# Optimization experiments

Hardware: AMD Instinct MI355X
Metric: run time of the kernel (lower is better)

## Reference

```python
import jax, jax.numpy as jnp
import numpy as np

B, S, F = 4, 2048, 1024
D_K = 1024


def setup_inputs() -> dict:
    key = jax.random.key(0)
    ks = jax.random.split(key, 9)
    s_in = 1.0 / np.sqrt(F)
    s_dk = 1.0 / np.sqrt(D_K)
    return {
        "x": jax.random.normal(ks[0], (B, S, F), jnp.float32),
        "Wq": jax.random.normal(ks[1], (F, D_K), jnp.float32) * s_in,
        "bq": jax.random.normal(ks[2], (D_K,), jnp.float32) * s_in,
        "Wk": jax.random.normal(ks[3], (F, D_K), jnp.float32) * s_in,
        "bk": jax.random.normal(ks[4], (D_K,), jnp.float32) * s_in,
        "Wv": jax.random.normal(ks[5], (F, D_K), jnp.float32) * s_in,
        "bv": jax.random.normal(ks[6], (D_K,), jnp.float32) * s_in,
        "Wo": jax.random.normal(ks[7], (D_K, F), jnp.float32) * s_dk,
        "bo": jax.random.normal(ks[8], (F,), jnp.float32) * s_dk,
    }


def reference(x, Wq, bq, Wk, bk, Wv, bv, Wo, bo):
    d_k = Wq.shape[1]
    # init_keys(x): keys/values are projections of the same sequence
    keys = jnp.einsum("bsf,fd->bsd", x, Wk) + bk      # [B,S,d_k]
    values = jnp.einsum("bsf,fd->bsd", x, Wv) + bv    # [B,S,d_k]
    queries = jnp.einsum("bsf,fd->bsd", x, Wq) + bq   # [B,S,d_k]
    # scores[b, q, k] = <queries[b,q], keys[b,k]> / sqrt(d_k)
    scores = jnp.einsum("bqd,bkd->bqk", queries, keys) / jnp.sqrt(
        jnp.asarray(d_k, x.dtype)
    )
    # NOTE: original softmaxes over dim=-2, i.e. over the QUERY axis
    attn = jax.nn.softmax(scores, axis=-2)            # [B,Sq,Sk]
    ctx = jnp.einsum("bqk,bkd->bqd", attn, values)    # [B,S,d_k]
    out = jnp.einsum("bqd,df->bqf", ctx, Wo) + bo     # [B,S,F]
    return out
```

## Files before the change

### kernel.cpp

```cpp
#include <hip/hip_runtime.h>
#include <hip/hip_bf16.h>
#include <cstdint>

typedef __bf16 bf16_t;
typedef __bf16 bf16x8 __attribute__((ext_vector_type(8)));
typedef float  floatx4 __attribute__((ext_vector_type(4)));

typedef const __attribute__((address_space(1))) unsigned int* gptr_t;
typedef __attribute__((address_space(3))) unsigned int* lptr_t;

static __device__ __forceinline__ void gl2lds16(const bf16_t* g, bf16_t* l) {
  __builtin_amdgcn_global_load_lds((gptr_t)g, (lptr_t)l, 16, 0, 0);
}

#define BAR()   asm volatile("s_barrier" ::: "memory")
#define WLGKM() asm volatile("s_waitcnt lgkmcnt(0)" ::: "memory")

template<int HAS_BIAS, int EXP_COLSUM, int SPLIT3>
__global__ __launch_bounds__(512, 2)
void gemm256(const bf16_t* __restrict__ A, const bf16_t* __restrict__ Bt,
             void* __restrict__ Cv,
             const float* __restrict__ b0, const float* __restrict__ b1,
             const float* __restrict__ b2,
             float* __restrict__ L,
             int M, int N, int K, int ldC, float alpha,
             long sA, long sB, long sC,
             long co0, long co1, long co2,
             int mbShift, int ldTv, long sTv)
{
  __shared__ __align__(16) char smemc[131072];

  const int bz = blockIdx.z;
  A  += bz * sA;
  Bt += bz * sB;

  int bx, by;
  {
    const int gx = gridDim.x, gy = gridDim.y;
    const int nwg = gx * gy;
    int id = blockIdx.x + gx * blockIdx.y;
    const int q = nwg >> 3, r = nwg & 7;
    const int xcd = id & 7, o = id >> 3;
    id = (xcd < r ? xcd * (q + 1) : r * (q + 1) + (xcd - r) * q) + o;
    bx = id % gx;
    by = id / gx;
  }

  const int gn0 = bx * 256;
  const int m0  = by * 256;
  const int tid  = threadIdx.x;
  const int lane = tid & 63;
  const int wave = tid >> 6;
  const int wm   = wave >> 2;
  const int wn   = wave & 3;
  const int lm   = lane & 15;
  const int quad = lane >> 4;

  int n0 = gn0, which = 0;
  bf16_t* Cb = (bf16_t*)Cv;
  const float* bias = b0;
  if (SPLIT3) {
    which = gn0 >> 10;
    n0 = gn0 & 1023;
    Cb += (which == 0) ? co0 : (which == 1) ? co1 : co2;
    bias = (which == 0) ? b0 : (which == 1) ? b1 : b2;
  }

  const int srow = tid >> 2;
  const int scol = ((tid ^ (tid >> 3)) & 3) * 8;
  const bf16_t* pA = A  + (long)(m0  + srow) * K + scol;
  const bf16_t* pB = Bt + (long)(gn0 + srow) * K + scol;

  const int nt = K >> 6;

  auto STAGE = [&](int s) {
    if (s >= 4 * nt) return;
    const int ts  = s >> 2;
    const int h   = s & 3;
    const int isA = h & 1;
    const int kh  = h >> 1;
    const bf16_t* gp = (isA ? pA : pB) + ts * 64 + kh * 32;
    char* lp = smemc + (ts & 1) * 65536 + (isA ? 0 : 32768) + kh * 16384
             + tid * 16;
    gl2lds16(gp,                (bf16_t*)lp);
    gl2lds16(gp + (long)128 * K, (bf16_t*)(lp + 8192));
  };

  const int csz  = ((quad ^ (lm >> 1)) & 3) * 16;
  const int aoff = (wm * 128 + lm) * 64 + csz;
  const int boff = (wn * 64  + lm) * 64 + csz;
  auto LDA = [&](int buf, int ks, int f) {
    return *(const bf16x8*)(smemc + buf * 65536 + ks * 16384 + aoff + f * 1024);
  };
  auto LDB = [&](int buf, int ks, int j) {
    return *(const bf16x8*)(smemc + buf * 65536 + 32768 + ks * 16384 + boff
                            + j * 1024);
  };

  floatx4 acc[8][4];
#pragma unroll
  for (int f = 0; f < 8; ++f)
#pragma unroll
    for (int j = 0; j < 4; ++j)
      acc[f][j] = (floatx4)(0.f);

#pragma unroll
  for (int s = 0; s < 7; ++s) STAGE(s);
  asm volatile("s_waitcnt vmcnt(6)" ::: "memory");
  BAR();

  for (int t = 0; t < nt; ++t) {
    const int buf = t & 1;
    bf16x8 a[4], b0r[4], b1r[4];

#pragma unroll
    for (int j = 0; j < 4; ++j) b0r[j] = LDB(buf, 0, j);
#pragma unroll
    for (int f = 0; f < 4; ++f) a[f] = LDA(buf, 0, f);
    STAGE(4 * t + 7);
    BAR(); WLGKM();
    __builtin_amdgcn_s_setprio(1);
#pragma unroll
    for (int f = 0; f < 4; ++f)
#pragma unroll
      for (int j = 0; j < 4; ++j)
        acc[f][j] = __builtin_amdgcn_mfma_f32_16x16x32_bf16(a[f], b0r[j],
                                                            acc[f][j], 0, 0, 0);
    __builtin_amdgcn_s_setprio(0);
    BAR();

#pragma unroll
    for (int j = 0; j < 4; ++j) b1r[j] = LDB(buf, 1, j);
#pragma unroll
    for (int f = 0; f < 4; ++f) a[f] = LDA(buf, 0, 4 + f);
    STAGE(4 * t + 8);
    BAR(); WLGKM();
    __builtin_amdgcn_s_setprio(1);
#pragma unroll
    for (int f = 0; f < 4; ++f)
#pragma unroll
      for (int j = 0; j < 4; ++j)
        acc[4 + f][j] = __builtin_amdgcn_mfma_f32_16x16x32_bf16(a[f], b0r[j],
                                                                acc[4 + f][j], 0, 0, 0);
    __builtin_amdgcn_s_setprio(0);
    BAR();

#pragma unroll
    for (int f = 0; f < 4; ++f) a[f] = LDA(buf, 1, f);
    STAGE(4 * t + 9);
    BAR(); WLGKM();
    __builtin_amdgcn_s_setprio(1);
#pragma unroll
    for (int f = 0; f < 4; ++f)
#pragma unroll
      for (int j = 0; j < 4; ++j)
        acc[f][j] = __builtin_amdgcn_mfma_f32_16x16x32_bf16(a[f], b1r[j],
                                                            acc[f][j], 0, 0, 0);
    __builtin_amdgcn_s_setprio(0);
    BAR();

#pragma unroll
    for (int f = 0; f < 4; ++f) a[f] = LDA(buf, 1, 4 + f);
    STAGE(4 * t + 10);
    BAR(); WLGKM();
    __builtin_amdgcn_s_setprio(1);
#pragma unroll
    for (int f = 0; f < 4; ++f)
#pragma unroll
      for (int j = 0; j < 4; ++j)
        acc[4 + f][j] = __builtin_amdgcn_mfma_f32_16x16x32_bf16(a[f], b1r[j],
                                                                acc[4 + f][j], 0, 0, 0);
    __builtin_amdgcn_s_setprio(0);
    if (t < nt - 2) { asm volatile("s_waitcnt vmcnt(6)" ::: "memory"); }
    else            { asm volatile("s_waitcnt vmcnt(0)" ::: "memory"); }
    BAR();
  }

  const int r8 = lane >> 3;
  const int c8 = lane & 7;

  if (SPLIT3 && which == 2) {
    bf16_t* myT = (bf16_t*)(smemc + wave * 4608);
    const int b  = m0 >> mbShift;
    const int s0 = m0 & ((1 << mbShift) - 1);
#pragma unroll
    for (int j = 0; j < 4; ++j) {
      const float bv = HAS_BIAS ? bias[n0 + wn * 64 + j * 16 + lm] : 0.f;
#pragma unroll
      for (int f = 0; f < 8; ++f)
#pragma unroll
        for (int r = 0; r < 4; ++r)
          myT[lm * 144 + f * 16 + quad * 4 + r] = (bf16_t)(acc[f][j][r] + bv);
#pragma unroll
      for (int t2 = 0; t2 < 4; ++t2) {
        const int dr = (t2 & 1) * 8 + r8;
        const int ck = (t2 >> 1) * 8 + c8;
        const bf16x8 vv = *(const bf16x8*)&myT[dr * 144 + ck * 8];
        *(bf16x8*)&Cb[(long)b * sTv + (long)(n0 + wn * 64 + j * 16 + dr) * ldTv
                      + s0 + wm * 128 + ck * 8] = vv;
      }
    }
  } else {
    bf16_t* myEp = (bf16_t*)(smemc + wave * 2176);
    float csum[4] = {0.f, 0.f, 0.f, 0.f};
    float bv[4];
#pragma unroll
    for (int j = 0; j < 4; ++j)
      bv[j] = HAS_BIAS ? bias[n0 + wn * 64 + j * 16 + lm] : 0.f;
#pragma unroll
    for (int f = 0; f < 8; ++f) {
#pragma unroll
      for (int j = 0; j < 4; ++j)
#pragma unroll
        for (int r = 0; r < 4; ++r) {
          float v = acc[f][j][r];
          if (EXP_COLSUM) { v = __expf(alpha * v); csum[j] += v; }
          v += bv[j];
          myEp[(quad * 4 + r) * 68 + j * 16 + lm] = (bf16_t)v;
        }
#pragma unroll
      for (int t2 = 0; t2 < 2; ++t2) {
        const int row = t2 * 8 + r8;
        const bf16x8 vv = *(const bf16x8*)&myEp[row * 68 + c8 * 8];
        *(bf16x8*)&Cb[bz * sC + (long)(m0 + wm * 128 + f * 16 + row) * ldC
                      + n0 + wn * 64 + c8 * 8] = vv;
      }
    }
    if (EXP_COLSUM) {
#pragma unroll
      for (int j = 0; j < 4; ++j) {
        float v = csum[j];
        v += __shfl_xor(v, 16);
        v += __shfl_xor(v, 32);
        if (quad == 0)
          atomicAdd(&L[bz * N + gn0 + wn * 64 + j * 16 + lm], v);
      }
    }
  }
}

template<int OUT_BF16, int HAS_BIAS, int EXP_COLSUM, int SPLIT3>
__global__ __launch_bounds__(256, 4)
void gemm_nt(const bf16_t* __restrict__ A, const bf16_t* __restrict__ Bt,
             void* __restrict__ Cv,
             const float* __restrict__ b0, const float* __restrict__ b1,
             const float* __restrict__ b2,
             float* __restrict__ L,
             int M, int N, int K, int ldC, float alpha,
             long sA, long sB, long sC,
             long co0, long co1, long co2,
             int mbShift, int ldTv, long sTv)
{
  __shared__ __align__(16) bf16_t smem[4 * 128 * 32];
  bf16_t* As0 = smem;
  bf16_t* Bs0 = smem + 4096;
  bf16_t* As1 = smem + 8192;
  bf16_t* Bs1 = smem + 12288;

  const int bz = blockIdx.z;
  A  += bz * sA;
  Bt += bz * sB;

  int bx = blockIdx.x, by = blockIdx.y;
  {
    const int gx = gridDim.x, gy = gridDim.y;
    const int nb = gx * gy;
    if (((nb & 7) == 0) && ((gx & 3) == 0) && ((gy & 7) == 0)) {
      const int id   = bx + gx * by;
      const int xcd  = id & 7;
      const int o    = id >> 3;
      const int rows = gy >> 3;
      const int pw   = rows << 2;
      const int p    = o / pw;
      const int r    = o - p * pw;
      by = xcd * rows + (r >> 2);
      bx = (p << 2) + (r & 3);
    }
  }

  const int gn0 = bx * 128;
  const int m0  = by * 128;
  const int tid  = threadIdx.x;
  const int lane = tid & 63;
  const int wave = tid >> 6;
  const int wm   = (wave >> 1) * 64;
  const int wn   = (wave & 1) * 64;
  const int lm   = lane & 15;
  const int quad = lane >> 4;

  int n0 = gn0;
  int which = 0;
  bf16_t* Cb = (bf16_t*)Cv;
  float*  Cf = (float*)Cv;
  const float* bias = b0;
  if (SPLIT3) {
    which = gn0 >> 10;
    n0 = gn0 & 1023;
    Cb += (which == 0) ? co0 : (which == 1) ? co1 : co2;
    bias = (which == 0) ? b0 : (which == 1) ? b1 : b2;
  }

  const int srow   = lane >> 2;
  const int schunk = (lane & 3) * 8;
  const int gchunk = ((lane & 3) ^ ((srow >> 1) & 3)) * 8;
  const int fswz   = ((lm >> 1) & 3) * 8;

  floatx4 acc[4][4];
#pragma unroll
  for (int i = 0; i < 4; ++i)
#pragma unroll
    for (int j = 0; j < 4; ++j)
      acc[i][j] = (floatx4)(0.f);

  for (int kk = 0; kk < K; kk += 64) {
    __syncthreads();
#pragma unroll
    for (int t = 0; t < 2; ++t) {
      const int r = wave * 32 + t * 16 + srow;
      const long ar = (long)(m0  + r) * K + kk + gchunk;
      const long br = (long)(gn0 + r) * K + kk + gchunk;
      gl2lds16(A  + ar,      &As0[r * 32 + schunk]);
      gl2lds16(A  + ar + 32, &As1[r * 32 + schunk]);
      gl2lds16(Bt + br,      &Bs0[r * 32 + schunk]);
      gl2lds16(Bt + br + 32, &Bs1[r * 32 + schunk]);
    }
    __syncthreads();

    {
      bf16x8 af[4], bfr[4];
#pragma unroll
      for (int i = 0; i < 4; ++i)
        af[i] = *(const bf16x8*)&As0[(wm + i * 16 + lm) * 32 + ((quad * 8) ^ fswz)];
#pragma unroll
      for (int j = 0; j < 4; ++j)
        bfr[j] = *(const bf16x8*)&Bs0[(wn + j * 16 + lm) * 32 + ((quad * 8) ^ fswz)];
#pragma unroll
      for (int i = 0; i < 4; ++i)
#pragma unroll
        for (int j = 0; j < 4; ++j)
          acc[i][j] = __builtin_amdgcn_mfma_f32_16x16x32_bf16(af[i], bfr[j],
                                                              acc[i][j], 0, 0, 0);
    }
    {
      bf16x8 af[4], bfr[4];
#pragma unroll
      for (int i = 0; i < 4; ++i)
        af[i] = *(const bf16x8*)&As1[(wm + i * 16 + lm) * 32 + ((quad * 8) ^ fswz)];
#pragma unroll
      for (int j = 0; j < 4; ++j)
        bfr[j] = *(const bf16x8*)&Bs1[(wn + j * 16 + lm) * 32 + ((quad * 8) ^ fswz)];
#pragma unroll
      for (int i = 0; i < 4; ++i)
#pragma unroll
        for (int j = 0; j < 4; ++j)
          acc[i][j] = __builtin_amdgcn_mfma_f32_16x16x32_bf16(af[i], bfr[j],
                                                              acc[i][j], 0, 0, 0);
    }
  }

  if (SPLIT3 && which == 2) {
    __syncthreads();
    bf16_t* myT = smem + wave * (16 * 68);
    const int b  = m0 >> mbShift;
    const int s0 = m0 & ((1 << mbShift) - 1);
    const int r8 = lane >> 3;
    const int c8 = lane & 7;
#pragma unroll
    for (int j = 0; j < 4; ++j) {
      const float bv = HAS_BIAS ? bias[n0 + wn + j * 16 + lm] : 0.f;
#pragma unroll
      for (int i = 0; i < 4; ++i)
#pragma unroll
        for (int r = 0; r < 4; ++r)
          myT[lm * 68 + i * 16 + quad * 4 + r] = (bf16_t)(acc[i][j][r] + bv);
#pragma unroll
      for (int t = 0; t < 2; ++t) {
        const int nr = t * 8 + r8;
        const bf16x8 vv = *(const bf16x8*)&myT[nr * 68 + c8 * 8];
        *(bf16x8*)&Cb[(long)b * sTv + (long)(n0 + wn + j * 16 + nr) * ldTv
                      + s0 + wm + c8 * 8] = vv;
      }
    }
  } else if (OUT_BF16) {
    __syncthreads();
    bf16_t* myEp = smem + wave * (16 * 68);
    const int r8 = lane >> 3;
    const int c8 = lane & 7;
    float cs[4] = {0.f, 0.f, 0.f, 0.f};
#pragma unroll
    for (int i = 0; i < 4; ++i) {
#pragma unroll
      for (int j = 0; j < 4; ++j) {
        const float bv = HAS_BIAS ? bias[n0 + wn + j * 16 + lm] : 0.f;
#pragma unroll
        for (int r = 0; r < 4; ++r) {
          float v = alpha * acc[i][j][r];
          if (EXP_COLSUM) { v = __expf(v); cs[j] += v; }
          v += bv;
          myEp[(quad * 4 + r) * 68 + j * 16 + lm] = (bf16_t)v;
        }
      }
#pragma unroll
      for (int t = 0; t < 2; ++t) {
        const int row = t * 8 + r8;
        const bf16x8 vv = *(const bf16x8*)&myEp[row * 68 + c8 * 8];
        *(bf16x8*)&Cb[bz * sC + (long)(m0 + wm + i * 16 + row) * ldC
                      + n0 + wn + c8 * 8] = vv;
      }
    }
    if (EXP_COLSUM) {
#pragma unroll
      for (int j = 0; j < 4; ++j) {
        float v = cs[j];
        v += __shfl_xor(v, 16);
        v += __shfl_xor(v, 32);
        if (quad == 0)
          atomicAdd(&L[bz * N + gn0 + wn + j * 16 + lm], v);
      }
    }
  } else {
#pragma unroll
    for (int j = 0; j < 4; ++j) {
      const int cn = n0 + wn + j * 16 + lm;
      const float bv = HAS_BIAS ? bias[n0 + wn + j * 16 + lm] : 0.f;
#pragma unroll
      for (int i = 0; i < 4; ++i) {
        const int rbase = m0 + wm + i * 16 + quad * 4;
#pragma unroll
        for (int r = 0; r < 4; ++r)
          Cf[bz * sC + (long)(rbase + r) * ldC + cn] = alpha * acc[i][j][r] + bv;
      }
    }
  }
}

__global__ __launch_bounds__(256)
void prep(const float* __restrict__ x, bf16_t* __restrict__ Xb,
          const float* __restrict__ w0, const float* __restrict__ w1,
          const float* __restrict__ w2, const float* __restrict__ w3,
          bf16_t* __restrict__ outQKV, bf16_t* __restrict__ outO)
{
  __shared__ float tile[32][33];
  const int id = blockIdx.x;
  if (id < 8192) {
    const long i = ((long)id * 256 + threadIdx.x) * 4;
    const float4 v = *(const float4*)(x + i);
    struct alignas(8) B4 { bf16_t a, b, c, d; };
    B4 o; o.a = (bf16_t)v.x; o.b = (bf16_t)v.y; o.c = (bf16_t)v.z; o.d = (bf16_t)v.w;
    *(B4*)(Xb + i) = o;
  } else {
    const int t = id - 8192;
    const int z = t >> 10;
    const int bx = t & 31, by = (t >> 5) & 31;
    const float* in = (z == 0) ? w0 : (z == 1) ? w1 : (z == 2) ? w2 : w3;
    bf16_t* out = (z < 3) ? outQKV + (long)z * 1024 * 1024 : outO;
    const int c0 = bx * 32, r0 = by * 32;
    const int tx = threadIdx.x & 31;
    const int ty = threadIdx.x >> 5;
#pragma unroll
    for (int i = 0; i < 32; i += 8)
      tile[ty + i][tx] = in[(long)(r0 + ty + i) * 1024 + (c0 + tx)];
    __syncthreads();
#pragma unroll
    for (int i = 0; i < 32; i += 8)
      out[(long)(c0 + ty + i) * 1024 + (r0 + tx)] = (bf16_t)tile[tx][ty + i];
  }
}

__global__ __launch_bounds__(256)
void scale_vt(bf16_t* __restrict__ Vt, const float* __restrict__ L, int S)
{
  const long base = ((long)blockIdx.x * blockDim.x + threadIdx.x) * 8;
  const int b  = (int)(base >> 21);
  const int s0 = (int)(base & (long)(S - 1));
  const float* Lb = L + b * S + s0;
  bf16x8 v = *(const bf16x8*)(Vt + base);
#pragma unroll
  for (int j = 0; j < 8; ++j)
    v[j] = (bf16_t)((float)v[j] / Lb[j]);
  *(bf16x8*)(Vt + base) = v;
}

extern "C" void kernel_launch(void* const* d_in, const int* in_sizes, int n_in,
                              void* d_out, int out_size, void* d_ws, size_t ws_size,
                              hipStream_t stream)
{
  const int Bz = 4, S = 2048, F = 1024, DK = 1024;
  const int M = Bz * S;

  const float* x  = (const float*)d_in[0];
  const float* Wq = (const float*)d_in[1];
  const float* bq = (const float*)d_in[2];
  const float* Wk = (const float*)d_in[3];
  const float* bk = (const float*)d_in[4];
  const float* Wv = (const float*)d_in[5];
  const float* bv = (const float*)d_in[6];
  const float* Wo = (const float*)d_in[7];
  const float* bo = (const float*)d_in[8];

  char* ws = (char*)d_ws;
  const size_t MB = 1ull << 20;
  bf16_t* Xb   = (bf16_t*)(ws + 0);
  bf16_t* Sc   = (bf16_t*)(ws + 0);
  bf16_t* Q    = (bf16_t*)(ws + 32 * MB);
  bf16_t* Ctx  = (bf16_t*)(ws + 32 * MB);
  bf16_t* Kb   = (bf16_t*)(ws + 48 * MB);
  bf16_t* Vt   = (bf16_t*)(ws + 64 * MB);
  bf16_t* WcatT= (bf16_t*)(ws + 80 * MB);
  float*  L    = (float*)(ws + 80 * MB);
  bf16_t* WoT  = (bf16_t*)(ws + 86 * MB);

  const long coQ = 16 * MB;
  const long coK = 24 * MB;
  const long coV = 32 * MB;

  prep<<<12288, 256, 0, stream>>>(x, Xb, Wq, Wk, Wv, Wo, WcatT, WoT);

  gemm256<1, 0, 1><<<dim3(3 * DK / 256, M / 256, 1), 512, 0, stream>>>(
      Xb, WcatT, (void*)ws, bq, bk, bv, nullptr, M, 3 * DK, F, DK, 1.f,
      0, 0, 0, coQ, coK, coV, 11, S, (long)DK * S);

  hipMemsetAsync(L, 0, (size_t)Bz * S * sizeof(float), stream);
  gemm256<0, 1, 0><<<dim3(S / 256, S / 256, Bz), 512, 0, stream>>>(
      Q, Kb, Sc, nullptr, nullptr, nullptr, L, S, S, DK, S, 0.03125f,
      (long)S * DK, (long)S * DK, (long)S * S, 0, 0, 0, 0, 0, 0);

  scale_vt<<<((long)Bz * DK * S / 8) / 256, 256, 0, stream>>>(Vt, L, S);

  gemm_nt<1, 0, 0, 0><<<dim3(DK / 128, S / 128, Bz), 256, 0, stream>>>(
      Sc, Vt, Ctx, nullptr, nullptr, nullptr, nullptr, S, DK, S, DK, 1.f,
      (long)S * S, (long)S * DK, (long)S * DK, 0, 0, 0, 0, 0, 0);

  gemm_nt<0, 1, 0, 0><<<dim3(F / 128, M / 128, 1), 256, 0, stream>>>(
      Ctx, WoT, d_out, bo, nullptr, nullptr, nullptr, M, F, DK, F, 1.f,
      0, 0, 0, 0, 0, 0, 0, 0, 0);
}
```

Before: 286.1 us.

## Restructure 256x256 GEMM main loop with register double-buffered LDS prefetch and grouped tile remap

Rewrites the gemm256 main loop as a manually unrolled pair-of-tiles schedule over eight separate LDS buffers. LDS-to-register fragment loads for the next phase are issued before the current MFMA batch, replacing lgkmcnt(0) waits with vmcnt-based waits, so LDS latency overlaps with matrix math. It also replaces the generic XCD block remap with a grouped mapping (4-column strips per XCD) meant to improve L2 reuse. The cost is higher register use from the extra fragment sets, more complex barrier and wait logic, and the new remap only applies when the grid dimensions divide evenly.

```diff
diff --git a/kernel.cpp b/kernel.cpp
--- a/kernel.cpp
+++ b/kernel.cpp
@@ -13,8 +13,22 @@
   __builtin_amdgcn_global_load_lds((gptr_t)g, (lptr_t)l, 16, 0, 0);
 }
 
-#define BAR()   asm volatile("s_barrier" ::: "memory")
-#define WLGKM() asm volatile("s_waitcnt lgkmcnt(0)" ::: "memory")
+#define BAR()     asm volatile("s_barrier" ::: "memory")
+#define VMW(NSTR) asm volatile("s_waitcnt vmcnt(" NSTR ")" ::: "memory")
+
+static __device__ __forceinline__ void mm16(floatx4 (&acc)[8][4], int R,
+                                            const bf16x8 (&A)[4],
+                                            const bf16x8 (&B)[4]) {
+  __builtin_amdgcn_s_setprio(1);
+#pragma unroll
+  for (int f = 0; f < 4; ++f)
+#pragma unroll
+    for (int j = 0; j < 4; ++j)
+      acc[R + f][j] = __builtin_amdgcn_mfma_f32_16x16x32_bf16(A[f], B[j],
+                                                              acc[R + f][j],
+                                                              0, 0, 0);
+  __builtin_amdgcn_s_setprio(0);
+}
 
 template<int HAS_BIAS, int EXP_COLSUM, int SPLIT3>
 __global__ __launch_bounds__(512, 2)
@@ -28,22 +42,34 @@
              long co0, long co1, long co2,
              int mbShift, int ldTv, long sTv)
 {
-  __shared__ __align__(16) char smemc[131072];
+  __shared__ __align__(16) bf16_t sA0k0[8192];
+  __shared__ __align__(16) bf16_t sA0k1[8192];
+  __shared__ __align__(16) bf16_t sB0k0[8192];
+  __shared__ __align__(16) bf16_t sB0k1[8192];
+  __shared__ __align__(16) bf16_t sA1k0[8192];
+  __shared__ __align__(16) bf16_t sA1k1[8192];
+  __shared__ __align__(16) bf16_t sB1k0[8192];
+  __shared__ __align__(16) bf16_t sB1k1[8192];
 
   const int bz = blockIdx.z;
   A  += bz * sA;
   Bt += bz * sB;
 
-  int bx, by;
+  int bx = blockIdx.x, by = blockIdx.y;
   {
     const int gx = gridDim.x, gy = gridDim.y;
-    const int nwg = gx * gy;
-    int id = blockIdx.x + gx * blockIdx.y;
-    const int q = nwg >> 3, r = nwg & 7;
-    const int xcd = id & 7, o = id >> 3;
-    id = (xcd < r ? xcd * (q + 1) : r * (q + 1) + (xcd - r) * q) + o;
-    bx = id % gx;
-    by = id / gx;
+    const int nb = gx * gy;
+    if (((nb & 7) == 0) && ((gx & 3) == 0) && ((gy & 7) == 0)) {
+      const int id   = bx + gx * by;
+      const int xcd  = id & 7;
+      const int o    = id >> 3;
+      const int rows = gy >> 3;
+      const int pw   = rows << 2;
+      const int p    = o / pw;
+      const int r    = o - p * pw;
+      by = xcd * rows + (r >> 2);
+      bx = (p << 2) + (r & 3);
+    }
   }
 
   const int gn0 = bx * 256;
@@ -73,29 +99,52 @@
 
   const int nt = K >> 6;
 
-  auto STAGE = [&](int s) {
-    if (s >= 4 * nt) return;
-    const int ts  = s >> 2;
-    const int h   = s & 3;
-    const int isA = h & 1;
-    const int kh  = h >> 1;
-    const bf16_t* gp = (isA ? pA : pB) + ts * 64 + kh * 32;
-    char* lp = smemc + (ts & 1) * 65536 + (isA ? 0 : 32768) + kh * 16384
-             + tid * 16;
-    gl2lds16(gp,                (bf16_t*)lp);
-    gl2lds16(gp + (long)128 * K, (bf16_t*)(lp + 8192));
-  };
-
-  const int csz  = ((quad ^ (lm >> 1)) & 3) * 16;
-  const int aoff = (wm * 128 + lm) * 64 + csz;
-  const int boff = (wn * 64  + lm) * 64 + csz;
-  auto LDA = [&](int buf, int ks, int f) {
-    return *(const bf16x8*)(smemc + buf * 65536 + ks * 16384 + aoff + f * 1024);
-  };
-  auto LDB = [&](int buf, int ks, int j) {
-    return *(const bf16x8*)(smemc + buf * 65536 + 32768 + ks * 16384 + boff
-                            + j * 1024);
-  };
+  const int csz_e = ((quad ^ (lm >> 1)) & 3) * 8;
+  const int aoffe = (wm * 128 + lm) * 32 + csz_e;
+  const int boffe = (wn * 64  + lm) * 32 + csz_e;
+
+#define STG(DST, GP) do { \
+    gl2lds16((GP), &DST[tid * 8]); \
+    gl2lds16((GP) + (long)128 * K, &DST[tid * 8 + 4096]); } while (0)
+
+#define LD4A(DSTR, ARR, FB) do { \
+    DSTR[0] = *(const bf16x8*)&ARR[aoffe + ((FB) + 0) * 512]; \
+    DSTR[1] = *(const bf16x8*)&ARR[aoffe + ((FB) + 1) * 512]; \
+    DSTR[2] = *(const bf16x8*)&ARR[aoffe + ((FB) + 2) * 512]; \
+    DSTR[3] = *(const bf16x8*)&ARR[aoffe + ((FB) + 3) * 512]; } while (0)
+
+#define LD4B(DSTR, ARR) do { \
+    DSTR[0] = *(const bf16x8*)&ARR[boffe + 0 * 512]; \
+    DSTR[1] = *(const bf16x8*)&ARR[boffe + 1 * 512]; \
+    DSTR[2] = *(const bf16x8*)&ARR[boffe + 2 * 512]; \
+    DSTR[3] = *(const bf16x8*)&ARR[boffe + 3 * 512]; } while (0)
+
+#define TILE8(AK0, AK1, BK0, BK1, OAK0, OAK1, OBK0, T, S0, S1, S2, S3, W0S, W2S, PF3) do { \
+     \
+    LD4A(qa, AK0, 4); \
+    if (S0) STG(OAK1, pA + ((T) + 1) * 64 + 32); \
+    BAR(); \
+    mm16(acc, 0, ra, rb); \
+    VMW(W0S); BAR(); \
+     \
+    LD4B(sb, BK1); LD4A(sa, AK1, 0); \
+    if (S1) STG(BK0, pB + ((T) + 2) * 64); \
+    BAR(); \
+    mm16(acc, 4, qa, rb); \
+    BAR(); \
+     \
+    LD4A(qa, AK1, 4); \
+    if (S2) STG(AK0, pA + ((T) + 2) * 64); \
+    BAR(); \
+    mm16(acc, 0, sa, sb); \
+    VMW(W2S); BAR(); \
+     \
+    if (PF3) { LD4B(rb, OBK0); LD4A(ra, OAK0, 0); } \
+    if (S3) STG(BK1, pB + ((T) + 2) * 64 + 32); \
+    BAR(); \
+    mm16(acc, 4, qa, sb); \
+    BAR(); \
+  } while (0)
 
   floatx4 acc[8][4];
 #pragma unroll
@@ -104,83 +153,36 @@
     for (int j = 0; j < 4; ++j)
       acc[f][j] = (floatx4)(0.f);
 
-#pragma unroll
-  for (int s = 0; s < 7; ++s) STAGE(s);
-  asm volatile("s_waitcnt vmcnt(6)" ::: "memory");
-  BAR();
-
-  for (int t = 0; t < nt; ++t) {
-    const int buf = t & 1;
-    bf16x8 a[4], b0r[4], b1r[4];
-
-#pragma unroll
-    for (int j = 0; j < 4; ++j) b0r[j] = LDB(buf, 0, j);
-#pragma unroll
-    for (int f = 0; f < 4; ++f) a[f] = LDA(buf, 0, f);
-    STAGE(4 * t + 7);
-    BAR(); WLGKM();
-    __builtin_amdgcn_s_setprio(1);
-#pragma unroll
-    for (int f = 0; f < 4; ++f)
-#pragma unroll
-      for (int j = 0; j < 4; ++j)
-        acc[f][j] = __builtin_amdgcn_mfma_f32_16x16x32_bf16(a[f], b0r[j],
-                                                            acc[f][j], 0, 0, 0);
-    __builtin_amdgcn_s_setprio(0);
-    BAR();
-
-#pragma unroll
-    for (int j = 0; j < 4; ++j) b1r[j] = LDB(buf, 1, j);
-#pragma unroll
-    for (int f = 0; f < 4; ++f) a[f] = LDA(buf, 0, 4 + f);
-    STAGE(4 * t + 8);
-    BAR(); WLGKM();
-    __builtin_amdgcn_s_setprio(1);
-#pragma unroll
-    for (int f = 0; f < 4; ++f)
-#pragma unroll
-      for (int j = 0; j < 4; ++j)
-        acc[4 + f][j] = __builtin_amdgcn_mfma_f32_16x16x32_bf16(a[f], b0r[j],
-                                                                acc[4 + f][j], 0, 0, 0);
-    __builtin_amdgcn_s_setprio(0);
-    BAR();
-
-#pragma unroll
-    for (int f = 0; f < 4; ++f) a[f] = LDA(buf, 1, f);
-    STAGE(4 * t + 9);
-    BAR(); WLGKM();
-    __builtin_amdgcn_s_setprio(1);
-#pragma unroll
-    for (int f = 0; f < 4; ++f)
-#pragma unroll
-      for (int j = 0; j < 4; ++j)
-        acc[f][j] = __builtin_amdgcn_mfma_f32_16x16x32_bf16(a[f], b1r[j],
-                                                            acc[f][j], 0, 0, 0);
-    __builtin_amdgcn_s_setprio(0);
-    BAR();
-
-#pragma unroll
-    for (int f = 0; f < 4; ++f) a[f] = LDA(buf, 1, 4 + f);
-    STAGE(4 * t + 10);
-    BAR(); WLGKM();
-    __builtin_amdgcn_s_setprio(1);
-#pragma unroll
-    for (int f = 0; f < 4; ++f)
-#pragma unroll
-      for (int j = 0; j < 4; ++j)
-        acc[4 + f][j] = __builtin_amdgcn_mfma_f32_16x16x32_bf16(a[f], b1r[j],
-                                                                acc[4 + f][j], 0, 0, 0);
-    __builtin_amdgcn_s_setprio(0);
-    if (t < nt - 2) { asm volatile("s_waitcnt vmcnt(6)" ::: "memory"); }
-    else            { asm volatile("s_waitcnt vmcnt(0)" ::: "memory"); }
-    BAR();
-  }
-
+  bf16x8 ra[4], rb[4], qa[4], sa[4], sb[4];
+
+  STG(sB0k0, pB);
+  STG(sA0k0, pA);
+  STG(sB0k1, pB + 32);
+  STG(sA0k1, pA + 32);
+  STG(sB1k0, pB + 64);
+  STG(sA1k0, pA + 64);
+  STG(sB1k1, pB + 96);
+  VMW("10"); BAR();
+  LD4B(rb, sB0k0);
+  LD4A(ra, sA0k0, 0);
+
+  const int npair = nt >> 1;
+  for (int p = 0; p < npair - 1; ++p) {
+    const int t0 = 2 * p;
+    TILE8(sA0k0, sA0k1, sB0k0, sB0k1, sA1k0, sA1k1, sB1k0, t0,     1, 1, 1, 1, "8", "8", 1);
+    TILE8(sA1k0, sA1k1, sB1k0, sB1k1, sA0k0, sA0k1, sB0k0, t0 + 1, 1, 1, 1, 1, "8", "8", 1);
+  }
+  TILE8(sA0k0, sA0k1, sB0k0, sB0k1, sA1k0, sA1k1, sB1k0, nt - 2, 1, 0, 0, 0, "8", "4", 1);
+  TILE8(sA1k0, sA1k1, sB1k0, sB1k1, sA0k0, sA0k1, sB0k0, nt - 1, 0, 0, 0, 0, "0", "0", 0);
+
+  __syncthreads();
   const int r8 = lane >> 3;
   const int c8 = lane & 7;
 
   if (SPLIT3 && which == 2) {
-    bf16_t* myT = (bf16_t*)(smemc + wave * 4608);
+    bf16_t* myT = (wave < 3) ? (sA0k0 + wave * 2304)
+                : (wave < 6) ? (sA0k1 + (wave - 3) * 2304)
+                             : (sB0k0 + (wave - 6) * 2304);
     const int b  = m0 >> mbShift;
     const int s0 = m0 & ((1 << mbShift) - 1);
 #pragma unroll
@@ -201,7 +203,7 @@
       }
     }
   } else {
-    bf16_t* myEp = (bf16_t*)(smemc + wave * 2176);
+    bf16_t* myEp = (wave < 7) ? (sA0k0 + wave * 1088) : sA0k1;
     float csum[4] = {0.f, 0.f, 0.f, 0.f};
     float bv[4];
 #pragma unroll
@@ -237,6 +239,10 @@
       }
     }
   }
+#undef STG
+#undef LD4A
+#undef LD4B
+#undef TILE8
 }
 
 template<int OUT_BF16, int HAS_BIAS, int EXP_COLSUM, int SPLIT3>
```

Result: slower. 292.0 us (+2.1%).
